# Performance work log

Measured on AMD Instinct MI355X. Metric: run time of the kernel, lower is better.

Reference implementation:

```python
import jax, jax.numpy as jnp
import numpy as np

N = 8192
IN_C = 512
OUT_C = 512


def setup_inputs() -> dict:
    key = jax.random.key(0)
    k1, k2, k3 = jax.random.split(key, 3)
    x = jax.random.normal(k1, (N, IN_C), dtype=jnp.float32)
    adj = jax.random.uniform(k2, (N, N), dtype=jnp.float32)
    # torch.rand initializer for the weight (uniform [0,1))
    w = jax.random.uniform(k3, (IN_C, OUT_C), dtype=jnp.float32)
    return {"x": x, "adj": adj, "w": w}


def reference(x, adj, w):
    # A = adj + I
    A = adj + jnp.eye(adj.shape[0], dtype=adj.dtype)
    # D_hat = diag(deg)^{-1/2}; diagonal inverse + sqrt == elementwise rsqrt of degrees
    deg = jnp.sum(A, axis=1)                      # [N]
    d_inv_sqrt = jax.lax.rsqrt(deg)               # [N]
    # A_hat = D_hat @ A @ D_hat == row/col scaling (same math, no dense inverse)
    A_hat = A * d_inv_sqrt[:, None] * d_inv_sqrt[None, :]
    mm_1 = A_hat @ x                              # [N, in_c]
    return jax.nn.elu(mm_1 @ w)                   # [N, out_c]
```

## Files before the change

### kernel.cpp

```cpp
#include <hip/hip_runtime.h>

#define NN 8192
#define CC 512

typedef __attribute__((ext_vector_type(8))) short short8;
typedef __attribute__((ext_vector_type(4))) float f32x4;
typedef unsigned short ushort_t;

__device__ __forceinline__ unsigned short f2bf(float f) {
    unsigned int u = __float_as_uint(f);
    u += 0x7FFF + ((u >> 16) & 1);
    return (unsigned short)(u >> 16);
}

__device__ __forceinline__ void gload_lds16(const void* g, void* l) {
    __builtin_amdgcn_global_load_lds((const __attribute__((address_space(1))) unsigned int*)g,
                                     (__attribute__((address_space(3))) unsigned int*)l,
                                     16, 0, 0);
}

__global__ __launch_bounds__(256) void k_rowsum_cvt(const float* __restrict__ adj,
                                                    float* __restrict__ ds,
                                                    ushort_t* __restrict__ adj16) {
    int row = blockIdx.x;
    const float4* p = (const float4*)(adj + (size_t)row * NN);
    ushort4* q = (ushort4*)(adj16 + (size_t)row * NN);
    float s = 0.f;
#pragma unroll
    for (int i = 0; i < 8; ++i) {
        float4 v = p[threadIdx.x + i * 256];
        s += (v.x + v.y) + (v.z + v.w);
        ushort4 u;
        u.x = f2bf(v.x); u.y = f2bf(v.y); u.z = f2bf(v.z); u.w = f2bf(v.w);
        q[threadIdx.x + i * 256] = u;
    }
#pragma unroll
    for (int off = 32; off > 0; off >>= 1) s += __shfl_down(s, off, 64);
    __shared__ float partial[4];
    if ((threadIdx.x & 63) == 0) partial[threadIdx.x >> 6] = s;
    __syncthreads();
    if (threadIdx.x == 0) {
        float deg = ((partial[0] + partial[1]) + (partial[2] + partial[3])) + 1.0f;
        ds[row] = rsqrtf(deg);
    }
}

__global__ __launch_bounds__(256) void k_rowsum(const float* __restrict__ adj,
                                                float* __restrict__ ds) {
    int row = blockIdx.x;
    const float4* p = (const float4*)(adj + (size_t)row * NN);
    float s = 0.f;
#pragma unroll
    for (int i = 0; i < 8; ++i) {
        float4 v = p[threadIdx.x + i * 256];
        s += (v.x + v.y) + (v.z + v.w);
    }
#pragma unroll
    for (int off = 32; off > 0; off >>= 1) s += __shfl_down(s, off, 64);
    __shared__ float partial[4];
    if ((threadIdx.x & 63) == 0) partial[threadIdx.x >> 6] = s;
    __syncthreads();
    if (threadIdx.x == 0) {
        float deg = ((partial[0] + partial[1]) + (partial[2] + partial[3])) + 1.0f;
        ds[row] = rsqrtf(deg);
    }
}

__global__ __launch_bounds__(256) void k_transpose(const float* __restrict__ in,
                                                   ushort_t* __restrict__ out,
                                                   const float* __restrict__ scale,
                                                   int R, int C) {
    __shared__ float tile[64][65];
    int r0 = blockIdx.x * 64, c0 = blockIdx.y * 64;
    int t = threadIdx.x;
    int cl = t & 63;
    int rl0 = t >> 6;
#pragma unroll
    for (int i = 0; i < 16; ++i) {
        int r = rl0 + i * 4;
        float v = in[(size_t)(r0 + r) * C + c0 + cl];
        float sc = scale ? scale[r0 + r] : 1.0f;
        tile[r][cl] = v * sc;
    }
    __syncthreads();
#pragma unroll
    for (int i = 0; i < 16; ++i) {
        int c = rl0 + i * 4;
        int r = cl;
        out[(size_t)(c0 + c) * R + r0 + r] = f2bf(tile[r][c]);
    }
}

__global__ __launch_bounds__(256, 4) void k_gemm1b(const ushort_t* __restrict__ adj16,
                                                   const ushort_t* __restrict__ yt,
                                                   float* __restrict__ part) {
    __shared__ __align__(16) ushort_t As[128 * 64];
    __shared__ __align__(16) ushort_t Bs[128 * 64];

    int t = threadIdx.x;
    int wid = t >> 6, lane = t & 63;

    int gid = blockIdx.x;
    int xcd = gid & 7, slot = gid >> 3;
    int cb = slot & 3;
    int g = (slot >> 2) * 8 + xcd;
    int rb = g & 63, ks = g >> 6;
    int rowBase = rb * 128, colBase = cb * 128;
    int kt0 = ks * (NN / 64 / 4), ktN = kt0 + NN / 64 / 4;

    int srow0 = t >> 3, ss = t & 7;

    f32x4 acc[4][4] = {};
    int wr = wid >> 1, wc = wid & 1;
    int fr = lane & 15, fq = lane >> 4;

    for (int kt = kt0; kt < ktN; ++kt) {
#pragma unroll
        for (int j = 0; j < 4; ++j) {
            int row = j * 32 + srow0;
            gload_lds16((const char*)(adj16 + (size_t)(rowBase + row) * NN + kt * 64 +
                                      ((ss ^ (row & 7)) << 3)),
                        (char*)As + j * 4096 + wid * 1024);
            gload_lds16((const char*)(yt + (size_t)(colBase + row) * NN + kt * 64 +
                                      ((ss ^ (row & 7)) << 3)),
                        (char*)Bs + j * 4096 + wid * 1024);
        }
        __syncthreads();
#pragma unroll
        for (int ks2 = 0; ks2 < 2; ++ks2) {
            short8 af[4], bf[4];
#pragma unroll
            for (int m = 0; m < 4; ++m) {
                int row = wr * 64 + m * 16 + fr;
                af[m] = *(const short8*)((const char*)As + row * 128 +
                                         ((ks2 * 64 + fq * 16) ^ ((row & 7) << 4)));
            }
#pragma unroll
            for (int n = 0; n < 4; ++n) {
                int col = wc * 64 + n * 16 + fr;
                bf[n] = *(const short8*)((const char*)Bs + col * 128 +
                                         ((ks2 * 64 + fq * 16) ^ ((col & 7) << 4)));
            }
#pragma unroll
            for (int m = 0; m < 4; ++m)
#pragma unroll
                for (int n = 0; n < 4; ++n)
                    acc[m][n] = __builtin_amdgcn_mfma_f32_16x16x32_bf16(af[m], bf[n], acc[m][n], 0, 0, 0);
        }
        __syncthreads();
    }

#pragma unroll
    for (int m = 0; m < 4; ++m) {
#pragma unroll
        for (int j = 0; j < 4; ++j) {
            int gr = rowBase + wr * 64 + m * 16 + fq * 4 + j;
#pragma unroll
            for (int n = 0; n < 4; ++n) {
                int gc = colBase + wc * 64 + n * 16 + fr;
                part[((size_t)ks * NN + gr) * CC + gc] = acc[m][n][j];
            }
        }
    }
}

template <int MODE>
__global__ __launch_bounds__(256, 4) void k_gemm1(const float* __restrict__ adj,
                                                  const ushort_t* __restrict__ yt,
                                                  const float* __restrict__ ds,
                                                  const float* __restrict__ x,
                                                  ushort_t* __restrict__ mm1,
                                                  float* __restrict__ part) {
    __shared__ __align__(16) ushort_t As[128 * 64];
    __shared__ __align__(16) ushort_t Bs[128 * 64];

    int t = threadIdx.x;
    int wid = t >> 6, lane = t & 63;

    int rowBase, colBase, kt0, ktN, ks;
    if (MODE == 0) {
        int bid = blockIdx.x;
        bid = (bid & 7) * 32 + (bid >> 3);
        colBase = (bid & 3) * 128;
        rowBase = (bid >> 2) * 128;
        kt0 = 0; ktN = NN / 64; ks = 0;
    } else {
        int gid = blockIdx.x;
        int xcd = gid & 7, slot = gid >> 3;
        int cb = slot & 3;
        int g = (slot >> 2) * 8 + xcd;
        int rb = g & 63; ks = g >> 6;
        rowBase = rb * 128; colBase = cb * 128;
        kt0 = ks * (NN / 64 / 4); ktN = kt0 + NN / 64 / 4;
    }

    int ar = t >> 4;
    int ac4 = t & 15;
    const float* aptr = adj + (size_t)(rowBase + ar) * NN + ac4 * 4;
    int brow0 = t >> 3;
    int bs = t & 7;

    float4 areg[8];

    auto loadA = [&](int kt) {
        const float* p = aptr + kt * 64;
#pragma unroll
        for (int i = 0; i < 8; ++i)
            areg[i] = *(const float4*)(p + (size_t)i * 16 * NN);
    };
    auto writeA = [&]() {
#pragma unroll
        for (int i = 0; i < 8; ++i) {
            int row = i * 16 + ar;
            ushort4 u;
            u.x = f2bf(areg[i].x); u.y = f2bf(areg[i].y);
            u.z = f2bf(areg[i].z); u.w = f2bf(areg[i].w);
            *(ushort4*)((char*)As + row * 128 + ((ac4 * 8) ^ ((row & 7) << 4))) = u;
        }
    };
    auto stageB = [&](int kt) {
#pragma unroll
        for (int j = 0; j < 4; ++j) {
            int row = j * 32 + brow0;
            gload_lds16((const char*)(yt + (size_t)(colBase + row) * NN + kt * 64 +
                                      ((bs ^ (row & 7)) << 3)),
                        (char*)Bs + j * 4096 + wid * 1024);
        }
    };

    f32x4 acc[4][4] = {};
    int wr = wid >> 1, wc = wid & 1;
    int fr = lane & 15, fq = lane >> 4;

    loadA(kt0);
    for (int kt = kt0; kt < ktN; ++kt) {
        writeA();
        stageB(kt);
        __syncthreads();
        if (kt + 1 < ktN) loadA(kt + 1);
#pragma unroll
        for (int ks2 = 0; ks2 < 2; ++ks2) {
            short8 af[4], bf[4];
#pragma unroll
            for (int m = 0; m < 4; ++m) {
                int row = wr * 64 + m * 16 + fr;
                af[m] = *(const short8*)((const char*)As + row * 128 +
                                         ((ks2 * 64 + fq * 16) ^ ((row & 7) << 4)));
            }
#pragma unroll
            for (int n = 0; n < 4; ++n) {
                int col = wc * 64 + n * 16 + fr;
                bf[n] = *(const short8*)((const char*)Bs + col * 128 +
                                         ((ks2 * 64 + fq * 16) ^ ((col & 7) << 4)));
            }
#pragma unroll
            for (int m = 0; m < 4; ++m)
#pragma unroll
                for (int n = 0; n < 4; ++n)
                    acc[m][n] = __builtin_amdgcn_mfma_f32_16x16x32_bf16(af[m], bf[n], acc[m][n], 0, 0, 0);
        }
        __syncthreads();
    }

#pragma unroll
    for (int m = 0; m < 4; ++m) {
#pragma unroll
        for (int j = 0; j < 4; ++j) {
            int gr = rowBase + wr * 64 + m * 16 + fq * 4 + j;
            float dsr = (MODE == 0) ? ds[gr] : 0.f;
#pragma unroll
            for (int n = 0; n < 4; ++n) {
                int gc = colBase + wc * 64 + n * 16 + fr;
                float p = acc[m][n][j];
                if (MODE == 0) {
                    float v = dsr * (p + dsr * x[(size_t)gr * CC + gc]);
                    mm1[(size_t)gr * CC + gc] = f2bf(v);
                } else {
                    part[((size_t)ks * NN + gr) * CC + gc] = p;
                }
            }
        }
    }
}

__global__ __launch_bounds__(256) void k_finish(const float* __restrict__ part,
                                                const float* __restrict__ ds,
                                                const float* __restrict__ x,
                                                ushort_t* __restrict__ mm1,
                                                int nsplit) {
    size_t i = (size_t)blockIdx.x * 256 + threadIdx.x;
    const f32x4* p = (const f32x4*)part;
    const size_t stride = (size_t)NN * CC / 4;
    f32x4 s = p[i];
    for (int k = 1; k < nsplit; ++k) s += p[i + (size_t)k * stride];
    int row = (int)(i >> 7);
    float d = ds[row];
    f32x4 xv = ((const f32x4*)x)[i];
    ushort4 u;
    u.x = f2bf(d * (s[0] + d * xv[0]));
    u.y = f2bf(d * (s[1] + d * xv[1]));
    u.z = f2bf(d * (s[2] + d * xv[2]));
    u.w = f2bf(d * (s[3] + d * xv[3]));
    ((ushort4*)mm1)[i] = u;
}

__global__ __launch_bounds__(256, 2) void k_gemm2(const ushort_t* __restrict__ mm1,
                                                  const ushort_t* __restrict__ wt,
                                                  float* __restrict__ out) {
    __shared__ __align__(16) ushort_t As[128 * 64];
    __shared__ __align__(16) ushort_t Bs[128 * 64];

    int t = threadIdx.x;
    int wid = t >> 6, lane = t & 63;
    int bid = blockIdx.x;
    bid = (bid & 7) * 32 + (bid >> 3);
    int cb = bid & 3, rb = bid >> 2;
    int rowBase = rb * 128, colBase = cb * 128;

    int srow0 = t >> 3, ss = t & 7;

    f32x4 acc[4][4] = {};
    int wr = wid >> 1, wc = wid & 1;
    int fr = lane & 15, fq = lane >> 4;

    for (int kt = 0; kt < CC / 64; ++kt) {
#pragma unroll
        for (int j = 0; j < 4; ++j) {
            int row = j * 32 + srow0;
            gload_lds16((const char*)(mm1 + (size_t)(rowBase + row) * CC + kt * 64 +
                                      ((ss ^ (row & 7)) << 3)),
                        (char*)As + j * 4096 + wid * 1024);
            gload_lds16((const char*)(wt + (size_t)(colBase + row) * CC + kt * 64 +
                                      ((ss ^ (row & 7)) << 3)),
                        (char*)Bs + j * 4096 + wid * 1024);
        }
        __syncthreads();
#pragma unroll
        for (int ks = 0; ks < 2; ++ks) {
            short8 af[4], bf[4];
#pragma unroll
            for (int m = 0; m < 4; ++m) {
                int row = wr * 64 + m * 16 + fr;
                af[m] = *(const short8*)((const char*)As + row * 128 +
                                         ((ks * 64 + fq * 16) ^ ((row & 7) << 4)));
            }
#pragma unroll
            for (int n = 0; n < 4; ++n) {
                int col = wc * 64 + n * 16 + fr;
                bf[n] = *(const short8*)((const char*)Bs + col * 128 +
                                         ((ks * 64 + fq * 16) ^ ((col & 7) << 4)));
            }
#pragma unroll
            for (int m = 0; m < 4; ++m)
#pragma unroll
                for (int n = 0; n < 4; ++n)
                    acc[m][n] = __builtin_amdgcn_mfma_f32_16x16x32_bf16(af[m], bf[n], acc[m][n], 0, 0, 0);
        }
        __syncthreads();
    }

#pragma unroll
    for (int m = 0; m < 4; ++m) {
#pragma unroll
        for (int j = 0; j < 4; ++j) {
            int gr = rowBase + wr * 64 + m * 16 + fq * 4 + j;
#pragma unroll
            for (int n = 0; n < 4; ++n) {
                int gc = colBase + wc * 64 + n * 16 + fr;
                float v = acc[m][n][j];
                out[(size_t)gr * CC + gc] = v > 0.f ? v : expm1f(v);
            }
        }
    }
}

extern "C" void kernel_launch(void* const* d_in, const int* in_sizes, int n_in,
                              void* d_out, int out_size, void* d_ws, size_t ws_size,
                              hipStream_t stream) {
    const float* x   = (const float*)d_in[0];
    const float* adj = (const float*)d_in[1];
    const float* w   = (const float*)d_in[2];
    float* out = (float*)d_out;

    char* ws = (char*)d_ws;
    size_t off = 0;
    float*    ds  = (float*)(ws + off);  off += 32u << 10;
    ushort_t* yt  = (ushort_t*)(ws + off);  off += 8u << 20;
    ushort_t* wt  = (ushort_t*)(ws + off);  off += 512u << 10;
    ushort_t* mm1 = (ushort_t*)(ws + off);  off += 8u << 20;
    float*    part = (float*)(ws + off);
    const size_t partBytes = 4 * (size_t)NN * CC * 4;
    ushort_t* adj16 = (ushort_t*)(ws + off + partBytes);
    const size_t adjBytes = (size_t)NN * NN * 2;

    if (ws_size >= off + partBytes + adjBytes) {
        k_rowsum_cvt<<<NN, 256, 0, stream>>>(adj, ds, adj16);
        k_transpose<<<dim3(NN / 64, CC / 64), 256, 0, stream>>>(x, yt, ds, NN, CC);
        k_transpose<<<dim3(CC / 64, CC / 64), 256, 0, stream>>>(w, wt, nullptr, CC, CC);
        k_gemm1b<<<1024, 256, 0, stream>>>(adj16, yt, part);
        k_finish<<<NN * CC / 4 / 256, 256, 0, stream>>>(part, ds, x, mm1, 4);
    } else if (ws_size >= off + partBytes) {
        k_rowsum<<<NN, 256, 0, stream>>>(adj, ds);
        k_transpose<<<dim3(NN / 64, CC / 64), 256, 0, stream>>>(x, yt, ds, NN, CC);
        k_transpose<<<dim3(CC / 64, CC / 64), 256, 0, stream>>>(w, wt, nullptr, CC, CC);
        k_gemm1<1><<<1024, 256, 0, stream>>>(adj, yt, ds, x, mm1, part);
        k_finish<<<NN * CC / 4 / 256, 256, 0, stream>>>(part, ds, x, mm1, 4);
    } else {
        k_rowsum<<<NN, 256, 0, stream>>>(adj, ds);
        k_transpose<<<dim3(NN / 64, CC / 64), 256, 0, stream>>>(x, yt, ds, NN, CC);
        k_transpose<<<dim3(CC / 64, CC / 64), 256, 0, stream>>>(w, wt, nullptr, CC, CC);
        k_gemm1<0><<<256, 256, 0, stream>>>(adj, yt, ds, x, mm1, part);
    }

    k_gemm2<<<256, 256, 0, stream>>>(mm1, wt, out);
}
```

Before: 228.8 us.

## Use 256x256 tiles with double-buffered LDS in the bf16 split-K GEMM

```diff
diff --git a/kernel.cpp b/kernel.cpp
--- a/kernel.cpp
+++ b/kernel.cpp
@@ -91,74 +91,83 @@
     }
 }
 
-__global__ __launch_bounds__(256, 4) void k_gemm1b(const ushort_t* __restrict__ adj16,
+__global__ __launch_bounds__(512, 2) void k_gemm1c(const ushort_t* __restrict__ adj16,
                                                    const ushort_t* __restrict__ yt,
                                                    float* __restrict__ part) {
-    __shared__ __align__(16) ushort_t As[128 * 64];
-    __shared__ __align__(16) ushort_t Bs[128 * 64];
+    __shared__ __align__(16) ushort_t As[2][256 * 32];
+    __shared__ __align__(16) ushort_t Bs[2][256 * 32];
 
     int t = threadIdx.x;
     int wid = t >> 6, lane = t & 63;
 
     int gid = blockIdx.x;
     int xcd = gid & 7, slot = gid >> 3;
-    int cb = slot & 3;
-    int g = (slot >> 2) * 8 + xcd;
-    int rb = g & 63, ks = g >> 6;
-    int rowBase = rb * 128, colBase = cb * 128;
-    int kt0 = ks * (NN / 64 / 4), ktN = kt0 + NN / 64 / 4;
-
-    int srow0 = t >> 3, ss = t & 7;
-
-    f32x4 acc[4][4] = {};
-    int wr = wid >> 1, wc = wid & 1;
+    int cb = slot & 1;
+    int u = (slot >> 1) + 16 * xcd;
+    int rb = u & 31, ks = u >> 5;
+    int rowBase = rb * 256, colBase = cb * 256;
+    int kt0 = ks * 64, ktN = kt0 + 64;
+
+    int wr = wid >> 2, wc = wid & 3;
     int fr = lane & 15, fq = lane >> 4;
 
+    int row0 = t >> 2, c0 = t & 3;
+    int sw0 = (c0 ^ (row0 & 3)) << 3;
+    const ushort_t* aSrc0 = adj16 + (size_t)(rowBase + row0) * NN + sw0;
+    const ushort_t* aSrc1 = adj16 + (size_t)(rowBase + row0 + 128) * NN + sw0;
+    const ushort_t* bSrc0 = yt + (size_t)(colBase + row0) * NN + sw0;
+    const ushort_t* bSrc1 = yt + (size_t)(colBase + row0 + 128) * NN + sw0;
+
+    auto stage = [&](int buf, int kt) {
+        int ko = kt * 32;
+        gload_lds16(aSrc0 + ko, (char*)As[buf] + wid * 1024);
+        gload_lds16(aSrc1 + ko, (char*)As[buf] + 8192 + wid * 1024);
+        gload_lds16(bSrc0 + ko, (char*)Bs[buf] + wid * 1024);
+        gload_lds16(bSrc1 + ko, (char*)Bs[buf] + 8192 + wid * 1024);
+    };
+
+    f32x4 acc[8][4] = {};
+    int sws = (fq ^ (fr & 3)) << 4;
+
+    stage(0, kt0);
+    __syncthreads();
+    int cur = 0;
     for (int kt = kt0; kt < ktN; ++kt) {
+        if (kt + 1 < ktN) stage(cur ^ 1, kt + 1);
+        const char* Ab = (const char*)As[cur];
+        const char* Bb = (const char*)Bs[cur];
+        short8 af[8], bfr[4];
+#pragma unroll
+        for (int m = 0; m < 8; ++m) {
+            int row = wr * 128 + m * 16 + fr;
+            af[m] = *(const short8*)(Ab + row * 64 + sws);
+        }
+#pragma unroll
+        for (int n = 0; n < 4; ++n) {
+            int col = wc * 64 + n * 16 + fr;
+            bfr[n] = *(const short8*)(Bb + col * 64 + sws);
+        }
+        __builtin_amdgcn_s_setprio(1);
+#pragma unroll
+        for (int m = 0; m < 8; ++m)
+#pragma unroll
+            for (int n = 0; n < 4; ++n)
+                acc[m][n] = __builtin_amdgcn_mfma_f32_16x16x32_bf16(af[m], bfr[n], acc[m][n], 0, 0, 0);
+        __builtin_amdgcn_s_setprio(0);
+        __syncthreads();
+        cur ^= 1;
+    }
+
+#pragma unroll
+    for (int m = 0; m < 8; ++m) {
 #pragma unroll
         for (int j = 0; j < 4; ++j) {
-            int row = j * 32 + srow0;
-            gload_lds16((const char*)(adj16 + (size_t)(rowBase + row) * NN + kt * 64 +
-                                      ((ss ^ (row & 7)) << 3)),
-                        (char*)As + j * 4096 + wid * 1024);
-            gload_lds16((const char*)(yt + (size_t)(colBase + row) * NN + kt * 64 +
-                                      ((ss ^ (row & 7)) << 3)),
-                        (char*)Bs + j * 4096 + wid * 1024);
-        }
-        __syncthreads();
-#pragma unroll
-        for (int ks2 = 0; ks2 < 2; ++ks2) {
-            short8 af[4], bf[4];
-#pragma unroll
-            for (int m = 0; m < 4; ++m) {
-                int row = wr * 64 + m * 16 + fr;
-                af[m] = *(const short8*)((const char*)As + row * 128 +
-                                         ((ks2 * 64 + fq * 16) ^ ((row & 7) << 4)));
-            }
-#pragma unroll
-            for (int n = 0; n < 4; ++n) {
-                int col = wc * 64 + n * 16 + fr;
-                bf[n] = *(const short8*)((const char*)Bs + col * 128 +
-                                         ((ks2 * 64 + fq * 16) ^ ((col & 7) << 4)));
-            }
-#pragma unroll
-            for (int m = 0; m < 4; ++m)
-#pragma unroll
-                for (int n = 0; n < 4; ++n)
-                    acc[m][n] = __builtin_amdgcn_mfma_f32_16x16x32_bf16(af[m], bf[n], acc[m][n], 0, 0, 0);
-        }
-        __syncthreads();
-    }
-
-#pragma unroll
-    for (int m = 0; m < 4; ++m) {
-#pragma unroll
-        for (int j = 0; j < 4; ++j) {
-            int gr = rowBase + wr * 64 + m * 16 + fq * 4 + j;
+            int gr = rowBase + wr * 128 + m * 16 + fq * 4 + j;
+            float* dst = &part[((size_t)ks * NN + gr) * CC];
 #pragma unroll
             for (int n = 0; n < 4; ++n) {
                 int gc = colBase + wc * 64 + n * 16 + fr;
-                part[((size_t)ks * NN + gr) * CC + gc] = acc[m][n][j];
+                dst[gc] = acc[m][n][j];
             }
         }
     }
@@ -397,7 +406,7 @@
         k_rowsum_cvt<<<NN, 256, 0, stream>>>(adj, ds, adj16);
         k_transpose<<<dim3(NN / 64, CC / 64), 256, 0, stream>>>(x, yt, ds, NN, CC);
         k_transpose<<<dim3(CC / 64, CC / 64), 256, 0, stream>>>(w, wt, nullptr, CC, CC);
-        k_gemm1b<<<1024, 256, 0, stream>>>(adj16, yt, part);
+        k_gemm1c<<<256, 512, 0, stream>>>(adj16, yt, part);
         k_finish<<<NN * CC / 4 / 256, 256, 0, stream>>>(part, ds, x, mm1, 4);
     } else if (ws_size >= off + partBytes) {
         k_rowsum<<<NN, 256, 0, stream>>>(adj, ds);
```

Result: no change. 229.9 us (+0.5%).
